# Kernel tuning notes

Hardware: AMD Instinct MI355X
Metric: run time of the kernel (lower is better)

Reference implementation:

```python
import jax, jax.numpy as jnp
import numpy as np

B, C, P, T = 256, 248, 50, 4
H = 8
D = C // H          # 31, used for the attention scale (self.d ** -0.5)
DH = D * T          # 124 == dim_head of RelPosEmb1DAISummer
FFD = 16
EPS = 1e-5


def _bn(x, g, b):
    # BatchNorm2d with batch statistics over (N, H, W) per channel
    m = x.mean(axis=(0, 2, 3), keepdims=True)
    v = x.var(axis=(0, 2, 3), keepdims=True)
    return (x - m) * jax.lax.rsqrt(v + EPS) * g[None, :, None, None] + b[None, :, None, None]


def _conv(x, w, b, pw):
    # kernel is (1, kw): 'same' padding only along the last (t) axis
    y = jax.lax.conv_general_dilated(x, w, (1, 1), ((0, 0), (pw, pw)),
                                     dimension_numbers=('NCHW', 'OIHW', 'NCHW'))
    return y + b[None, :, None, None]


def _rel_to_abs(x):
    # x: [b, h, l, 2l-1] -> [b, h, l, l] (Bottleneck-Transformer trick)
    b, h, l, _ = x.shape
    x = jnp.pad(x, ((0, 0), (0, 0), (0, 0), (0, 1)))           # b h l 2l
    x = x.reshape(b, h, 2 * l * l)
    x = jnp.pad(x, ((0, 0), (0, 0), (0, l - 1)))
    x = x.reshape(b, h, l + 1, 2 * l - 1)
    return x[:, :, :l, l - 1:]


def _forward(x, w_qkv, b_qkv, rel_emb, g1, beta1, w_c1, bc1, w_c2, bc2,
             g_cfe, beta_cfe, w_c3, bc3, g2, beta2):
    b, c, p, t = x.shape
    h, d = H, c // H
    dh = d * t
    # 1x1 conv qkv projection
    qkv = jnp.einsum('bcpt,oc->bopt', x, w_qkv) + b_qkv[None, :, None, None]
    qkv = qkv.reshape(b, 3, h, d, p, t)
    q = qkv[:, 0].transpose(0, 1, 3, 2, 4).reshape(b, h, p, dh)   # b h p (d t)
    k = qkv[:, 1].transpose(0, 1, 2, 4, 3).reshape(b, h, dh, p)   # b h (d t) p
    v = qkv[:, 2].transpose(0, 1, 3, 2, 4).reshape(b, h, p, dh)
    dots = jnp.matmul(q, k)                                       # b h p p
    bias = _rel_to_abs(jnp.einsum('bhpd,rd->bhpr', q, rel_emb))   # shared-head rel bias
    attn = jax.nn.softmax((dots + bias) * (d ** -0.5), axis=-1)   # scale AFTER bias, d=31
    out = jnp.matmul(attn, v)                                     # b h p dh
    out = out.reshape(b, h, p, d, t).transpose(0, 1, 3, 2, 4).reshape(b, c, p, t)
    # residual + BN1
    x = _bn(out + x, g1, beta1)
    # CFE: two parallel convs, concat, BN, ELU, 1x1 conv (dropout = identity, eval)
    y = jnp.concatenate([_conv(x, w_c1, bc1, 1), _conv(x, w_c2, bc2, 2)], axis=1)
    y = jax.nn.elu(_bn(y, g_cfe, beta_cfe))
    y = _conv(y, w_c3, bc3, 0)
    # residual + BN2
    return _bn(y + x, g2, beta2)


def setup_inputs() -> dict:
    key = jax.random.key(0)
    ks = jax.random.split(key, 8)
    rn = lambda k, sh, s=1.0: jax.random.normal(k, sh, dtype=jnp.float32) * s
    return dict(
        x=rn(ks[0], (B, C, P, T)),
        w_qkv=rn(ks[1], (3 * C, C), 0.05), b_qkv=jnp.zeros((3 * C,), jnp.float32),
        rel_emb=rn(ks[2], (2 * P - 1, DH), DH ** -0.5),
        g1=jnp.ones((C,), jnp.float32), beta1=jnp.zeros((C,), jnp.float32),
        w_c1=rn(ks[3], (FFD // 2, C, 1, 3), 0.05), bc1=jnp.zeros((FFD // 2,), jnp.float32),
        w_c2=rn(ks[4], (FFD // 2, C, 1, 5), 0.05), bc2=jnp.zeros((FFD // 2,), jnp.float32),
        g_cfe=jnp.ones((FFD,), jnp.float32), beta_cfe=jnp.zeros((FFD,), jnp.float32),
        w_c3=rn(ks[5], (C, FFD, 1, 1), 0.05), bc3=jnp.zeros((C,), jnp.float32),
        g2=jnp.ones((C,), jnp.float32), beta2=jnp.zeros((C,), jnp.float32),
    )


def reference(x, w_qkv, b_qkv, rel_emb, g1, beta1, w_c1, bc1, w_c2, bc2,
              g_cfe, beta_cfe, w_c3, bc3, g2, beta2):
    return _forward(x, w_qkv, b_qkv, rel_emb, g1, beta1, w_c1, bc1, w_c2, bc2,
                    g_cfe, beta_cfe, w_c3, bc3, g2, beta2)
```

## Files before the change

kernel.cpp:

```cpp
#include <hip/hip_runtime.h>

#define B_ 256
#define C_ 248
#define P_ 50
#define T_ 4
#define H_ 8
#define D_ 31
#define DH_ 124
#define PT_ 200
#define O3_ 744

typedef __attribute__((ext_vector_type(8))) short short8v;
typedef __attribute__((ext_vector_type(4))) float f32x4;

__device__ __forceinline__ float bf2f(unsigned short u) {
  union { unsigned int i; float f; } v; v.i = ((unsigned int)u) << 16; return v.f;
}
__device__ __forceinline__ unsigned short f2bf(float f) {
  union { float f; unsigned int i; } v; v.f = f;
  unsigned int r = v.i + 0x7fffu + ((v.i >> 16) & 1u);
  return (unsigned short)(r >> 16);
}

__global__ void relcvt_kernel(const float* __restrict__ rel, unsigned short* __restrict__ out) {
  int i = blockIdx.x * 256 + threadIdx.x;
  if (i < 112 * 128) {
    int r = i >> 7, k = i & 127;
    out[i] = (r < 99 && k < DH_) ? f2bf(rel[r * DH_ + k]) : (unsigned short)0;
  }
}

__global__ void wcvt_kernel(const float* __restrict__ w, unsigned short* __restrict__ wbf) {
  int i = blockIdx.x * 256 + threadIdx.x;
  if (i < 768 * 64) {
    int o = i >> 6, c = (i & 63) * 4;
    ushort4 val = make_ushort4(0, 0, 0, 0);
    if (o < O3_ && c < C_) {
      float4 wv = *(const float4*)(w + (size_t)o * C_ + c);
      val.x = f2bf(wv.x); val.y = f2bf(wv.y); val.z = f2bf(wv.z); val.w = f2bf(wv.w);
    }
    *(ushort4*)(wbf + (size_t)o * 256 + c) = val;
  }
}

__global__ __launch_bounds__(256) void xt_kernel(const float* __restrict__ x,
                                                 unsigned short* __restrict__ xT) {
  __shared__ float xs[64 * 65];
  const int tid = threadIdx.x;
  const int pt0 = (blockIdx.x & 3) * 64;
  const int c0 = (blockIdx.x >> 2) * 64;
  const int b = blockIdx.y;
#pragma unroll
  for (int pass = 0; pass < 4; ++pass) {
    int row = pass * 16 + (tid >> 4);
    int ptl4 = (tid & 15) * 4;
    int c = c0 + row, pt = pt0 + ptl4;
    float4 v = make_float4(0.f, 0.f, 0.f, 0.f);
    if (c < C_) {
      const float* src = x + ((size_t)b * C_ + c) * PT_ + pt;
      if (pt + 3 < PT_) v = *(const float4*)src;
      else {
        if (pt + 0 < PT_) v.x = src[0];
        if (pt + 1 < PT_) v.y = src[1];
        if (pt + 2 < PT_) v.z = src[2];
        if (pt + 3 < PT_) v.w = src[3];
      }
    }
    xs[row * 65 + ptl4 + 0] = v.x; xs[row * 65 + ptl4 + 1] = v.y;
    xs[row * 65 + ptl4 + 2] = v.z; xs[row * 65 + ptl4 + 3] = v.w;
  }
  __syncthreads();
#pragma unroll
  for (int pass = 0; pass < 4; ++pass) {
    int ptl = pass * 16 + (tid >> 4);
    int cl4 = (tid & 15) * 4;
    int pt = pt0 + ptl;
    if (pt < 208) {
      ushort4 pk;
      pk.x = f2bf(xs[(cl4 + 0) * 65 + ptl]);
      pk.y = f2bf(xs[(cl4 + 1) * 65 + ptl]);
      pk.z = f2bf(xs[(cl4 + 2) * 65 + ptl]);
      pk.w = f2bf(xs[(cl4 + 3) * 65 + ptl]);
      *(ushort4*)(xT + ((size_t)b * 208 + pt) * 256 + c0 + cl4) = pk;
    }
  }
}

__global__ __launch_bounds__(256) void fused_qa_kernel(
    const unsigned short* __restrict__ xT, const unsigned short* __restrict__ wbf,
    const float* __restrict__ bias, const unsigned short* __restrict__ relp,
    const float* __restrict__ x, float* __restrict__ pre1) {
  __shared__ __align__(16) unsigned short RA[64 * 128];
  __shared__ __align__(16) unsigned short RB[64 * 128];
  __shared__ __align__(16) unsigned short RC[128 * 64];
  const int tid = threadIdx.x;
  const int xcd = blockIdx.x & 7, slot = blockIdx.x >> 3;
  const int b = xcd * 32 + (slot >> 3), h = slot & 7;
  const unsigned short* xb = xT + (size_t)b * 208 * 256;
  const int w = tid >> 6, l = tid & 63;
  const int lr = l & 15, lk = (l >> 4) * 8;
  const int mstart = (w == 0) ? 0 : (1 + 3 * w);
  const int mcount = (w == 0) ? 4 : 3;
  const float scale = 0.17960530202677491f;

  {
    float4 z = make_float4(0.f, 0.f, 0.f, 0.f);
    float4* z1 = (float4*)RA; float4* z2 = (float4*)RB; float4* z3 = (float4*)RC;
    for (int i = tid; i < 1024; i += 256) { z1[i] = z; z2[i] = z; z3[i] = z; }
  }

  const f32x4 zf = {0.f, 0.f, 0.f, 0.f};
  f32x4 acc[4][6];
#pragma unroll
  for (int mi = 0; mi < 4; ++mi)
#pragma unroll
    for (int nt = 0; nt < 6; ++nt) acc[mi][nt] = zf;

#pragma unroll
  for (int ks = 0; ks < 8; ++ks) {
    int k0 = ks * 32 + lk;
    short8v bfr[6];
#pragma unroll
    for (int nt = 0; nt < 6; ++nt) {
      int orow = (nt >> 1) * 248 + h * 31 + (nt & 1) * 16 + lr;
      bfr[nt] = *(const short8v*)(wbf + (size_t)orow * 256 + k0);
    }
#pragma unroll
    for (int mi = 0; mi < 4; ++mi) {
      if (mi < mcount) {
        short8v a = *(const short8v*)(xb + (size_t)((mstart + mi) * 16 + lr) * 256 + k0);
#pragma unroll
        for (int nt = 0; nt < 6; ++nt)
          acc[mi][nt] = __builtin_amdgcn_mfma_f32_16x16x32_bf16(a, bfr[nt], acc[mi][nt], 0, 0, 0);
      }
    }
  }
  __syncthreads();
#pragma unroll
  for (int mi = 0; mi < 4; ++mi) {
    if (mi < mcount) {
      int p = (mstart + mi) * 4 + (l >> 4);
      if (p < P_) {
#pragma unroll
        for (int nt = 0; nt < 6; ++nt) {
          int d = (nt & 1) * 16 + lr;
          if (d < D_) {
            int wi = nt >> 1;
            float bo = bias[wi * C_ + h * D_ + d];
            f32x4 av = acc[mi][nt];
            if (wi == 2) {
#pragma unroll
              for (int r = 0; r < 4; ++r) {
                int dh = d * 4 + r;
                *(unsigned short*)((char*)RC + ((dh * 128 + p * 2) ^ ((dh & 7) << 4))) = f2bf(av[0] + bo);
                av = __builtin_shufflevector(av, av, 1, 2, 3, 0);
              }
            } else if (wi == 0) {
              ushort4 pk;
              pk.x = f2bf((av[0] + bo) * scale); pk.y = f2bf((av[1] + bo) * scale);
              pk.z = f2bf((av[2] + bo) * scale); pk.w = f2bf((av[3] + bo) * scale);
              *(ushort4*)((char*)RA + ((p * 256 + d * 8) ^ ((p & 7) << 4))) = pk;
            } else {
              ushort4 pk;
              pk.x = f2bf(av[0] + bo); pk.y = f2bf(av[1] + bo);
              pk.z = f2bf(av[2] + bo); pk.w = f2bf(av[3] + bo);
              *(ushort4*)((char*)RB + ((p * 256 + d * 8) ^ ((p & 7) << 4))) = pk;
            }
          }
        }
      }
    }
  }
  __syncthreads();

  const int arow = 16 * w + lr;
  const int prow0 = 16 * w + (l >> 4) * 4;

  f32x4 accS[4]; f32x4 accR[7];
#pragma unroll
  for (int n = 0; n < 4; ++n) accS[n] = zf;
#pragma unroll
  for (int n = 0; n < 7; ++n) accR[n] = zf;

#pragma unroll
  for (int ks = 0; ks < 4; ++ks) {
    int k0 = ks * 32 + lk;
    short8v a = *(const short8v*)((const char*)RA + ((arow * 256 + 2 * k0) ^ ((arow & 7) << 4)));
#pragma unroll
    for (int n = 0; n < 4; ++n) {
      int brow = 16 * n + lr;
      short8v bb = *(const short8v*)((const char*)RB + ((brow * 256 + 2 * k0) ^ ((brow & 7) << 4)));
      accS[n] = __builtin_amdgcn_mfma_f32_16x16x32_bf16(a, bb, accS[n], 0, 0, 0);
    }
#pragma unroll
    for (int n = 0; n < 7; ++n) {
      int rrow = 16 * n + lr;
      short8v bb = *(const short8v*)(relp + rrow * 128 + k0);
      accR[n] = __builtin_amdgcn_mfma_f32_16x16x32_bf16(a, bb, accR[n], 0, 0, 0);
    }
  }
  __syncthreads();

  unsigned short* bias_s = RB;
#pragma unroll
  for (int n = 0; n < 7; ++n)
#pragma unroll
    for (int r = 0; r < 4; ++r) {
      int p = prow0 + r;
      int j = 16 * n + lr - 49 + p;
      if (p < P_ && j >= 0 && j < P_)
        bias_s[p * 64 + j] = f2bf(accR[n][r]);
    }
  __syncthreads();

  float sv[4][4];
#pragma unroll
  for (int n = 0; n < 4; ++n)
#pragma unroll
    for (int r = 0; r < 4; ++r) {
      int p = prow0 + r, j = 16 * n + lr;
      if (p < P_ && j < P_)
        sv[n][r] = accS[n][r] + bf2f(bias_s[p * 64 + j]);
      else
        sv[n][r] = -1e30f;
    }
#pragma unroll
  for (int r = 0; r < 4; ++r) {
    float mm = fmaxf(fmaxf(sv[0][r], sv[1][r]), fmaxf(sv[2][r], sv[3][r]));
    mm = fmaxf(mm, __shfl_xor(mm, 1));
    mm = fmaxf(mm, __shfl_xor(mm, 2));
    mm = fmaxf(mm, __shfl_xor(mm, 4));
    mm = fmaxf(mm, __shfl_xor(mm, 8));
    float ss = 0.f;
#pragma unroll
    for (int n = 0; n < 4; ++n) { float e = __expf(sv[n][r] - mm); sv[n][r] = e; ss += e; }
    ss += __shfl_xor(ss, 1); ss += __shfl_xor(ss, 2);
    ss += __shfl_xor(ss, 4); ss += __shfl_xor(ss, 8);
    float inv = 1.f / ss;
#pragma unroll
    for (int n = 0; n < 4; ++n) sv[n][r] *= inv;
  }
#pragma unroll
  for (int n = 0; n < 4; ++n)
#pragma unroll
    for (int r = 0; r < 4; ++r) {
      int p = prow0 + r, j = 16 * n + lr;
      *(unsigned short*)((char*)RA + ((p * 128 + 2 * j) ^ ((p & 7) << 4))) = f2bf(sv[n][r]);
    }
  __syncthreads();

  f32x4 accO[8];
#pragma unroll
  for (int n = 0; n < 8; ++n) accO[n] = zf;
#pragma unroll
  for (int ks = 0; ks < 2; ++ks) {
    int j0 = ks * 32 + lk;
    short8v a = *(const short8v*)((const char*)RA + ((arow * 128 + 2 * j0) ^ ((arow & 7) << 4)));
#pragma unroll
    for (int n = 0; n < 8; ++n) {
      int vrow = 16 * n + lr;
      short8v bb = *(const short8v*)((const char*)RC + ((vrow * 128 + 2 * j0) ^ ((vrow & 7) << 4)));
      accO[n] = __builtin_amdgcn_mfma_f32_16x16x32_bf16(a, bb, accO[n], 0, 0, 0);
    }
  }
#pragma unroll
  for (int n = 0; n < 8; ++n) {
    int dh = 16 * n + lr;
    if (dh < DH_) {
      int c = h * D_ + (dh >> 2), t = dh & 3;
#pragma unroll
      for (int r = 0; r < 4; ++r) {
        int p = prow0 + r;
        if (p < P_) {
          size_t idx = (((size_t)b * C_ + c) * P_ + p) * T_ + t;
          pre1[idx] = accO[n][r] + x[idx];
        }
      }
    }
  }
}

__global__ __launch_bounds__(256) void bnstat_kernel(
    const float* __restrict__ t, const float* __restrict__ g, const float* __restrict__ be,
    float* __restrict__ a, float* __restrict__ bs, int nch) {
  const int c = blockIdx.x;
  const int tid = threadIdx.x;
  const float* base = t + ((size_t)tid * nch + c) * PT_;
  float s = 0.f, s2 = 0.f;
  for (int i = 0; i < PT_; i += 4) {
    float4 v = *(const float4*)(base + i);
    s += v.x + v.y + v.z + v.w;
    s2 += v.x*v.x + v.y*v.y + v.z*v.z + v.w*v.w;
  }
#pragma unroll
  for (int off = 32; off > 0; off >>= 1) {
    s += __shfl_down(s, off);
    s2 += __shfl_down(s2, off);
  }
  __shared__ float r1[4], r2[4];
  if ((tid & 63) == 0) { r1[tid>>6] = s; r2[tid>>6] = s2; }
  __syncthreads();
  if (tid == 0) {
    s = r1[0]+r1[1]+r1[2]+r1[3];
    s2 = r2[0]+r2[1]+r2[2]+r2[3];
    const float inv = 1.f / (float)(B_ * PT_);
    float m = s * inv;
    float var = s2 * inv - m * m;
    float ai = g[c] * rsqrtf(var + 1e-5f);
    a[c] = ai;
    bs[c] = be[c] - m * ai;
  }
}

__global__ __launch_bounds__(256) void p1t_kernel(const float* __restrict__ pre1,
                                                  unsigned short* __restrict__ p1T) {
  __shared__ float xs[64][205];
  const int b = blockIdx.x;
  const int tid = threadIdx.x;
  for (int c0 = 0; c0 < C_; c0 += 64) {
    int R = (C_ - c0 < 64) ? (C_ - c0) : 64;
    __syncthreads();
    for (int e = tid; e < R * 50; e += 256) {
      int row = e / 50, pq = e - (e / 50) * 50;
      float4 v = *(const float4*)(pre1 + ((size_t)b * C_ + c0 + row) * PT_ + pq * 4);
      xs[row][pq*4+0]=v.x; xs[row][pq*4+1]=v.y; xs[row][pq*4+2]=v.z; xs[row][pq*4+3]=v.w;
    }
    __syncthreads();
    for (int u = tid; u < 50 * R; u += 256) {
      int p = u / R, cl = u - (u / R) * R;
      ushort4 pk;
      pk.x = f2bf(xs[cl][p*4+0]); pk.y = f2bf(xs[cl][p*4+1]);
      pk.z = f2bf(xs[cl][p*4+2]); pk.w = f2bf(xs[cl][p*4+3]);
      *(ushort4*)(p1T + ((size_t)b*50 + p) * 1024 + (c0+cl)*4) = pk;
    }
  }
  for (int u = tid; u < 50 * 8; u += 256) {
    int p = u >> 3, g = u & 7;
    ushort4 val = make_ushort4(0,0,0,0);
    if (g == 0) val.x = 0x3F80;
    *(ushort4*)(p1T + ((size_t)b*50 + p) * 1024 + 992 + g*4) = val;
  }
}

__global__ __launch_bounds__(256) void wcfe_kernel(
    const float* __restrict__ w1, const float* __restrict__ bc1,
    const float* __restrict__ w2, const float* __restrict__ bc2,
    const float* __restrict__ a1, const float* __restrict__ b1,
    unsigned short* __restrict__ Wbig) {
  const int n = blockIdx.x;
  const int f = n >> 2, t = n & 3;
  const int tid = threadIdx.x;
  __shared__ float red[256];
  float partial = 0.f;
  if (tid < C_) {
    int c = tid;
    float tv[4];
    float tsum = 0.f;
#pragma unroll
    for (int tp = 0; tp < 4; ++tp) {
      int dt = tp - t;
      float v = 0.f;
      if (f < 8) { if (dt >= -1 && dt <= 1) v = w1[(f * C_ + c) * 3 + dt + 1]; }
      else       { if (dt >= -2 && dt <= 2) v = w2[((f - 8) * C_ + c) * 5 + dt + 2]; }
      tv[tp] = v; tsum += v;
    }
    float ac = a1[c];
#pragma unroll
    for (int tp = 0; tp < 4; ++tp)
      Wbig[n * 1024 + c * 4 + tp] = f2bf(ac * tv[tp]);
    partial = b1[c] * tsum;
  } else {
#pragma unroll
    for (int tp = 0; tp < 4; ++tp) {
      int col = tid * 4 + tp;
      if (col > 992 && col < 1024) Wbig[n * 1024 + col] = 0;
    }
  }
  red[tid] = partial;
  __syncthreads();
  for (int s = 128; s > 0; s >>= 1) {
    if (tid < s) red[tid] += red[tid + s];
    __syncthreads();
  }
  if (tid == 0) {
    float bias = (f < 8) ? bc1[f] : bc2[f - 8];
    Wbig[n * 1024 + 992] = f2bf(bias + red[0]);
  }
}

__global__ __launch_bounds__(256) void cfe12g_kernel(
    const unsigned short* __restrict__ p1T, const unsigned short* __restrict__ Wbig,
    float* __restrict__ y16) {
  const int tid = threadIdx.x;
  const int w = tid >> 6, l = tid & 63;
  const int lr = l & 15, lk = (l >> 4) * 8;
  const int m0 = blockIdx.x * 32;
  const f32x4 zf = {0.f, 0.f, 0.f, 0.f};
  f32x4 acc0 = zf, acc1 = zf;
  const unsigned short* wrow = Wbig + (size_t)(w * 16 + lr) * 1024;
#pragma unroll
  for (int ks = 0; ks < 32; ++ks) {
    int k0 = ks * 32 + lk;
    short8v bfr = *(const short8v*)(wrow + k0);
    short8v a0 = *(const short8v*)(p1T + (size_t)(m0 + lr) * 1024 + k0);
    short8v a1v = *(const short8v*)(p1T + (size_t)(m0 + 16 + lr) * 1024 + k0);
    acc0 = __builtin_amdgcn_mfma_f32_16x16x32_bf16(a0, bfr, acc0, 0, 0, 0);
    acc1 = __builtin_amdgcn_mfma_f32_16x16x32_bf16(a1v, bfr, acc1, 0, 0, 0);
  }
  const int n = w * 16 + lr, f = n >> 2, tt = n & 3;
#pragma unroll
  for (int mt = 0; mt < 2; ++mt) {
    f32x4 av = (mt == 0) ? acc0 : acc1;
#pragma unroll
    for (int r = 0; r < 4; ++r) {
      int m = m0 + mt * 16 + (l >> 4) * 4 + r;
      int b = m / 50, p = m - (m / 50) * 50;
      y16[((size_t)b * 16 + f) * PT_ + p * 4 + tt] = av[r];
    }
  }
}

__global__ __launch_bounds__(256) void cfe3_kernel(
    const float* __restrict__ y16, const float* __restrict__ ac, const float* __restrict__ bcf,
    const float* __restrict__ w3, const float* __restrict__ bc3,
    const float* __restrict__ pre1, const float* __restrict__ a1, const float* __restrict__ b1,
    float* __restrict__ pre2) {
  const int b = blockIdx.x;
  const int tid = threadIdx.x;
  __shared__ float zs[16][PT_];
  __shared__ float w3s[C_][16];
  for (int i = tid; i < C_*16; i += 256) w3s[i >> 4][i & 15] = w3[i];
  for (int e = tid; e < 16*PT_; e += 256) {
    int f = e / PT_, pt = e - f * PT_;
    float v = y16[((size_t)b*16 + f) * PT_ + pt] * ac[f] + bcf[f];
    zs[f][pt] = (v > 0.f) ? v : (__expf(v) - 1.f);
  }
  __syncthreads();
  for (int e = tid; e < C_ * P_; e += 256) {
    int c = e / P_, p = e - (e / P_) * P_;
    float b3 = bc3[c];
    float4 o = make_float4(b3, b3, b3, b3);
#pragma unroll
    for (int f = 0; f < 16; ++f) {
      float wv = w3s[c][f];
      float4 z = *(const float4*)&zs[f][p*4];
      o.x += wv * z.x; o.y += wv * z.y; o.z += wv * z.z; o.w += wv * z.w;
    }
    size_t idx = (((size_t)b * C_ + c) * P_ + p) * T_;
    float4 xr = *(const float4*)(pre1 + idx);
    float a1c = a1[c], b1c = b1[c];
    o.x += xr.x * a1c + b1c;
    o.y += xr.y * a1c + b1c;
    o.z += xr.z * a1c + b1c;
    o.w += xr.w * a1c + b1c;
    *(float4*)(pre2 + idx) = o;
  }
}

__global__ __launch_bounds__(256) void bnapply_kernel(
    const float* __restrict__ pre2, const float* __restrict__ a, const float* __restrict__ bs,
    float* __restrict__ out) {
  int i = blockIdx.x * 256 + threadIdx.x;
  if (i < (B_*C_*PT_)/4) {
    int row = (i * 4) / PT_;
    int c = row % C_;
    float4 v = *(const float4*)(pre2 + (size_t)i * 4);
    float ai = a[c], bi = bs[c];
    float4 o = make_float4(v.x*ai+bi, v.y*ai+bi, v.z*ai+bi, v.w*ai+bi);
    *(float4*)(out + (size_t)i * 4) = o;
  }
}

extern "C" void kernel_launch(void* const* d_in, const int* in_sizes, int n_in,
                              void* d_out, int out_size, void* d_ws, size_t ws_size,
                              hipStream_t stream) {
  const float* x        = (const float*)d_in[0];
  const float* w_qkv    = (const float*)d_in[1];
  const float* b_qkv    = (const float*)d_in[2];
  const float* rel      = (const float*)d_in[3];
  const float* g1       = (const float*)d_in[4];
  const float* beta1    = (const float*)d_in[5];
  const float* w_c1     = (const float*)d_in[6];
  const float* bc1      = (const float*)d_in[7];
  const float* w_c2     = (const float*)d_in[8];
  const float* bc2      = (const float*)d_in[9];
  const float* g_cfe    = (const float*)d_in[10];
  const float* beta_cfe = (const float*)d_in[11];
  const float* w_c3     = (const float*)d_in[12];
  const float* bc3      = (const float*)d_in[13];
  const float* g2       = (const float*)d_in[14];
  const float* beta2    = (const float*)d_in[15];
  float* out = (float*)d_out;
  char* ws = (char*)d_ws;

  unsigned short* xT    = (unsigned short*)(ws);
  unsigned short* wbf   = (unsigned short*)(ws + 27262976);
  unsigned short* p1T   = (unsigned short*)(ws + 27656192);
  float* pre1           = (float*)(ws + 76185600);
  float* y16            = (float*)(ws + 126976000);
  unsigned short* relp  = (unsigned short*)(ws + 130252800);
  unsigned short* Wbig  = (unsigned short*)(ws + 130281472);
  float* st             = (float*)(ws + 130412544);
  float* a1 = st, *b1 = st + 256, *acf = st + 512, *bcf = st + 544, *a2 = st + 576, *b2 = st + 832;
  float* pre2           = (float*)ws;

  relcvt_kernel<<<56, 256, 0, stream>>>(rel, relp);
  wcvt_kernel<<<192, 256, 0, stream>>>(w_qkv, wbf);
  xt_kernel<<<dim3(16, 256), 256, 0, stream>>>(x, xT);
  fused_qa_kernel<<<2048, 256, 0, stream>>>(xT, wbf, b_qkv, relp, x, pre1);
  bnstat_kernel<<<248, 256, 0, stream>>>(pre1, g1, beta1, a1, b1, C_);
  p1t_kernel<<<256, 256, 0, stream>>>(pre1, p1T);
  wcfe_kernel<<<64, 256, 0, stream>>>(w_c1, bc1, w_c2, bc2, a1, b1, Wbig);
  cfe12g_kernel<<<400, 256, 0, stream>>>(p1T, Wbig, y16);
  bnstat_kernel<<<16, 256, 0, stream>>>(y16, g_cfe, beta_cfe, acf, bcf, 16);
  cfe3_kernel<<<256, 256, 0, stream>>>(y16, acf, bcf, w_c3, bc3, pre1, a1, b1, pre2);
  bnstat_kernel<<<248, 256, 0, stream>>>(pre2, g2, beta2, a2, b2, C_);
  bnapply_kernel<<<12400, 256, 0, stream>>>(pre2, a2, b2, out);
}
```

Measured before the change: 397.8 us.

## Fuse BN1 stats and bf16 transpose into attention epilogue, split BN reductions

The attention kernel now writes its residual output straight into the bf16 transposed buffer and accumulates per-channel sum and sum-of-squares partials. This removes the fp32 pre1 tensor, the separate transpose kernel and the full BN1 statistics pass. cfe3 reads the residual back from the bf16 buffer instead of fp32, which lowers the precision of the residual path. The remaining BN statistics passes are split into a partial-reduction kernel over more blocks plus a small finalize kernel, to get more parallelism. The epilogue's stores are scattered 2-byte writes, which may coalesce poorly.

```diff
diff --git a/kernel.cpp b/kernel.cpp
--- a/kernel.cpp
+++ b/kernel.cpp
@@ -89,7 +89,8 @@
 __global__ __launch_bounds__(256) void fused_qa_kernel(
     const unsigned short* __restrict__ xT, const unsigned short* __restrict__ wbf,
     const float* __restrict__ bias, const unsigned short* __restrict__ relp,
-    const float* __restrict__ x, float* __restrict__ pre1) {
+    const float* __restrict__ x, unsigned short* __restrict__ p1T,
+    float* __restrict__ partial1) {
   __shared__ __align__(16) unsigned short RA[64 * 128];
   __shared__ __align__(16) unsigned short RB[64 * 128];
   __shared__ __align__(16) unsigned short RC[128 * 64];
@@ -263,6 +264,9 @@
       accO[n] = __builtin_amdgcn_mfma_f32_16x16x32_bf16(a, bb, accO[n], 0, 0, 0);
     }
   }
+  float psum[8], psq[8];
+#pragma unroll
+  for (int n = 0; n < 8; ++n) { psum[n] = 0.f; psq[n] = 0.f; }
 #pragma unroll
   for (int n = 0; n < 8; ++n) {
     int dh = 16 * n + lr;
@@ -272,37 +276,66 @@
       for (int r = 0; r < 4; ++r) {
         int p = prow0 + r;
         if (p < P_) {
-          size_t idx = (((size_t)b * C_ + c) * P_ + p) * T_ + t;
-          pre1[idx] = accO[n][r] + x[idx];
+          float val = accO[n][r] + x[(((size_t)b * C_ + c) * P_ + p) * T_ + t];
+          p1T[((size_t)b * 50 + p) * 1024 + h * DH_ + dh] = f2bf(val);
+          psum[n] += val;
+          psq[n] += val * val;
         }
       }
     }
   }
-}
-
-__global__ __launch_bounds__(256) void bnstat_kernel(
-    const float* __restrict__ t, const float* __restrict__ g, const float* __restrict__ be,
-    float* __restrict__ a, float* __restrict__ bs, int nch) {
+#pragma unroll
+  for (int n = 0; n < 8; ++n) {
+    psum[n] += __shfl_xor(psum[n], 1);  psq[n] += __shfl_xor(psq[n], 1);
+    psum[n] += __shfl_xor(psum[n], 2);  psq[n] += __shfl_xor(psq[n], 2);
+    psum[n] += __shfl_xor(psum[n], 16); psq[n] += __shfl_xor(psq[n], 16);
+    psum[n] += __shfl_xor(psum[n], 32); psq[n] += __shfl_xor(psq[n], 32);
+  }
+  float* fs = (float*)RB;
+  if ((l & 3) == 0 && l < 16) {
+    int g2 = l >> 2;
+#pragma unroll
+    for (int n = 0; n < 8; ++n) {
+      int d = 4 * n + g2;
+      if (d < D_) { fs[w * 32 + d] = psum[n]; fs[128 + w * 32 + d] = psq[n]; }
+    }
+  }
+  __syncthreads();
+  if (tid < D_) {
+    float s = fs[tid] + fs[32 + tid] + fs[64 + tid] + fs[96 + tid];
+    float s2 = fs[128 + tid] + fs[160 + tid] + fs[192 + tid] + fs[224 + tid];
+    partial1[((size_t)b * 8 + h) * 62 + tid] = s;
+    partial1[((size_t)b * 8 + h) * 62 + 31 + tid] = s2;
+  }
+  if (h == 7) {
+    for (int u = tid; u < 400; u += 256) {
+      int p = u >> 3, g3 = u & 7;
+      ushort4 vz = make_ushort4(0, 0, 0, 0);
+      if (g3 == 0) vz.x = 0x3F80;
+      *(ushort4*)(p1T + ((size_t)b * 50 + p) * 1024 + 992 + g3 * 4) = vz;
+    }
+  }
+}
+
+__global__ __launch_bounds__(256) void bnfin1_kernel(
+    const float* __restrict__ partial1, const float* __restrict__ g,
+    const float* __restrict__ be, float* __restrict__ a, float* __restrict__ bs) {
   const int c = blockIdx.x;
-  const int tid = threadIdx.x;
-  const float* base = t + ((size_t)tid * nch + c) * PT_;
-  float s = 0.f, s2 = 0.f;
-  for (int i = 0; i < PT_; i += 4) {
-    float4 v = *(const float4*)(base + i);
-    s += v.x + v.y + v.z + v.w;
-    s2 += v.x*v.x + v.y*v.y + v.z*v.z + v.w*v.w;
-  }
-#pragma unroll
-  for (int off = 32; off > 0; off >>= 1) {
-    s += __shfl_down(s, off);
-    s2 += __shfl_down(s2, off);
+  const int h = c / D_, d = c - h * D_;
+  const int tid = threadIdx.x;
+  const float* pp = partial1 + ((size_t)tid * 8 + h) * 62;
+  float s = pp[d], s2 = pp[31 + d];
+#pragma unroll
+  for (int off = 1; off <= 32; off <<= 1) {
+    s += __shfl_xor(s, off);
+    s2 += __shfl_xor(s2, off);
   }
   __shared__ float r1[4], r2[4];
-  if ((tid & 63) == 0) { r1[tid>>6] = s; r2[tid>>6] = s2; }
+  if ((tid & 63) == 0) { r1[tid >> 6] = s; r2[tid >> 6] = s2; }
   __syncthreads();
   if (tid == 0) {
-    s = r1[0]+r1[1]+r1[2]+r1[3];
-    s2 = r2[0]+r2[1]+r2[2]+r2[3];
+    s = r1[0] + r1[1] + r1[2] + r1[3];
+    s2 = r2[0] + r2[1] + r2[2] + r2[3];
     const float inv = 1.f / (float)(B_ * PT_);
     float m = s * inv;
     float var = s2 * inv - m * m;
@@ -312,33 +345,52 @@
   }
 }
 
-__global__ __launch_bounds__(256) void p1t_kernel(const float* __restrict__ pre1,
-                                                  unsigned short* __restrict__ p1T) {
-  __shared__ float xs[64][205];
-  const int b = blockIdx.x;
-  const int tid = threadIdx.x;
-  for (int c0 = 0; c0 < C_; c0 += 64) {
-    int R = (C_ - c0 < 64) ? (C_ - c0) : 64;
-    __syncthreads();
-    for (int e = tid; e < R * 50; e += 256) {
-      int row = e / 50, pq = e - (e / 50) * 50;
-      float4 v = *(const float4*)(pre1 + ((size_t)b * C_ + c0 + row) * PT_ + pq * 4);
-      xs[row][pq*4+0]=v.x; xs[row][pq*4+1]=v.y; xs[row][pq*4+2]=v.z; xs[row][pq*4+3]=v.w;
-    }
-    __syncthreads();
-    for (int u = tid; u < 50 * R; u += 256) {
-      int p = u / R, cl = u - (u / R) * R;
-      ushort4 pk;
-      pk.x = f2bf(xs[cl][p*4+0]); pk.y = f2bf(xs[cl][p*4+1]);
-      pk.z = f2bf(xs[cl][p*4+2]); pk.w = f2bf(xs[cl][p*4+3]);
-      *(ushort4*)(p1T + ((size_t)b*50 + p) * 1024 + (c0+cl)*4) = pk;
-    }
-  }
-  for (int u = tid; u < 50 * 8; u += 256) {
-    int p = u >> 3, g = u & 7;
-    ushort4 val = make_ushort4(0,0,0,0);
-    if (g == 0) val.x = 0x3F80;
-    *(ushort4*)(p1T + ((size_t)b*50 + p) * 1024 + 992 + g*4) = val;
+__global__ __launch_bounds__(256) void bnstat_part_kernel(
+    const float* __restrict__ t, float* __restrict__ part, int nch) {
+  const int c = blockIdx.x, g = blockIdx.y;
+  const int tid = threadIdx.x;
+  const int bsl = tid >> 3, k = tid & 7;
+  const int b = g * 32 + bsl;
+  const float* base = t + ((size_t)b * nch + c) * PT_;
+  float s = 0.f, s2 = 0.f;
+  for (int j = k; j < 50; j += 8) {
+    float4 v = *(const float4*)(base + j * 4);
+    s += v.x + v.y + v.z + v.w;
+    s2 += v.x * v.x + v.y * v.y + v.z * v.z + v.w * v.w;
+  }
+#pragma unroll
+  for (int off = 1; off <= 32; off <<= 1) {
+    s += __shfl_xor(s, off);
+    s2 += __shfl_xor(s2, off);
+  }
+  __shared__ float r1[4], r2[4];
+  if ((tid & 63) == 0) { r1[tid >> 6] = s; r2[tid >> 6] = s2; }
+  __syncthreads();
+  if (tid == 0) {
+    s = r1[0] + r1[1] + r1[2] + r1[3];
+    s2 = r2[0] + r2[1] + r2[2] + r2[3];
+    part[((size_t)c * 8 + g) * 2] = s;
+    part[((size_t)c * 8 + g) * 2 + 1] = s2;
+  }
+}
+
+__global__ __launch_bounds__(256) void bnfin_kernel(
+    const float* __restrict__ part, const float* __restrict__ g,
+    const float* __restrict__ be, float* __restrict__ a, float* __restrict__ bs, int nch) {
+  int c = threadIdx.x;
+  if (c < nch) {
+    float s = 0.f, s2 = 0.f;
+#pragma unroll
+    for (int gg = 0; gg < 8; ++gg) {
+      s += part[((size_t)c * 8 + gg) * 2];
+      s2 += part[((size_t)c * 8 + gg) * 2 + 1];
+    }
+    const float inv = 1.f / (float)(B_ * PT_);
+    float m = s * inv;
+    float var = s2 * inv - m * m;
+    float ai = g[c] * rsqrtf(var + 1e-5f);
+    a[c] = ai;
+    bs[c] = be[c] - m * ai;
   }
 }
 
@@ -423,16 +475,16 @@
 __global__ __launch_bounds__(256) void cfe3_kernel(
     const float* __restrict__ y16, const float* __restrict__ ac, const float* __restrict__ bcf,
     const float* __restrict__ w3, const float* __restrict__ bc3,
-    const float* __restrict__ pre1, const float* __restrict__ a1, const float* __restrict__ b1,
+    const unsigned short* __restrict__ p1T, const float* __restrict__ a1, const float* __restrict__ b1,
     float* __restrict__ pre2) {
   const int b = blockIdx.x;
   const int tid = threadIdx.x;
   __shared__ float zs[16][PT_];
   __shared__ float w3s[C_][16];
-  for (int i = tid; i < C_*16; i += 256) w3s[i >> 4][i & 15] = w3[i];
-  for (int e = tid; e < 16*PT_; e += 256) {
+  for (int i = tid; i < C_ * 16; i += 256) w3s[i >> 4][i & 15] = w3[i];
+  for (int e = tid; e < 16 * PT_; e += 256) {
     int f = e / PT_, pt = e - f * PT_;
-    float v = y16[((size_t)b*16 + f) * PT_ + pt] * ac[f] + bcf[f];
+    float v = y16[((size_t)b * 16 + f) * PT_ + pt] * ac[f] + bcf[f];
     zs[f][pt] = (v > 0.f) ? v : (__expf(v) - 1.f);
   }
   __syncthreads();
@@ -443,16 +495,16 @@
 #pragma unroll
     for (int f = 0; f < 16; ++f) {
       float wv = w3s[c][f];
-      float4 z = *(const float4*)&zs[f][p*4];
+      float4 z = *(const float4*)&zs[f][p * 4];
       o.x += wv * z.x; o.y += wv * z.y; o.z += wv * z.z; o.w += wv * z.w;
     }
+    ushort4 xr = *(const ushort4*)(p1T + ((size_t)(b * 50 + p)) * 1024 + c * 4);
+    float a1c = a1[c], b1c = b1[c];
+    o.x += bf2f(xr.x) * a1c + b1c;
+    o.y += bf2f(xr.y) * a1c + b1c;
+    o.z += bf2f(xr.z) * a1c + b1c;
+    o.w += bf2f(xr.w) * a1c + b1c;
     size_t idx = (((size_t)b * C_ + c) * P_ + p) * T_;
-    float4 xr = *(const float4*)(pre1 + idx);
-    float a1c = a1[c], b1c = b1[c];
-    o.x += xr.x * a1c + b1c;
-    o.y += xr.y * a1c + b1c;
-    o.z += xr.z * a1c + b1c;
-    o.w += xr.w * a1c + b1c;
     *(float4*)(pre2 + idx) = o;
   }
 }
@@ -461,12 +513,12 @@
     const float* __restrict__ pre2, const float* __restrict__ a, const float* __restrict__ bs,
     float* __restrict__ out) {
   int i = blockIdx.x * 256 + threadIdx.x;
-  if (i < (B_*C_*PT_)/4) {
+  if (i < (B_ * C_ * PT_) / 4) {
     int row = (i * 4) / PT_;
     int c = row % C_;
     float4 v = *(const float4*)(pre2 + (size_t)i * 4);
     float ai = a[c], bi = bs[c];
-    float4 o = make_float4(v.x*ai+bi, v.y*ai+bi, v.z*ai+bi, v.w*ai+bi);
+    float4 o = make_float4(v.x * ai + bi, v.y * ai + bi, v.z * ai + bi, v.w * ai + bi);
     *(float4*)(out + (size_t)i * 4) = o;
   }
 }
@@ -496,24 +548,27 @@
   unsigned short* xT    = (unsigned short*)(ws);
   unsigned short* wbf   = (unsigned short*)(ws + 27262976);
   unsigned short* p1T   = (unsigned short*)(ws + 27656192);
-  float* pre1           = (float*)(ws + 76185600);
+  float* part2          = (float*)(ws + 53870592);
+  float* partY          = (float*)(ws + 53886464);
+  float* pre2           = (float*)(ws + 76185600);
   float* y16            = (float*)(ws + 126976000);
+  float* partial1       = (float*)(ws + 126976000);
   unsigned short* relp  = (unsigned short*)(ws + 130252800);
   unsigned short* Wbig  = (unsigned short*)(ws + 130281472);
   float* st             = (float*)(ws + 130412544);
   float* a1 = st, *b1 = st + 256, *acf = st + 512, *bcf = st + 544, *a2 = st + 576, *b2 = st + 832;
-  float* pre2           = (float*)ws;
 
   relcvt_kernel<<<56, 256, 0, stream>>>(rel, relp);
   wcvt_kernel<<<192, 256, 0, stream>>>(w_qkv, wbf);
   xt_kernel<<<dim3(16, 256), 256, 0, stream>>>(x, xT);
-  fused_qa_kernel<<<2048, 256, 0, stream>>>(xT, wbf, b_qkv, relp, x, pre1);
-  bnstat_kernel<<<248, 256, 0, stream>>>(pre1, g1, beta1, a1, b1, C_);
-  p1t_kernel<<<256, 256, 0, stream>>>(pre1, p1T);
+  fused_qa_kernel<<<2048, 256, 0, stream>>>(xT, wbf, b_qkv, relp, x, p1T, partial1);
+  bnfin1_kernel<<<248, 256, 0, stream>>>(partial1, g1, beta1, a1, b1);
   wcfe_kernel<<<64, 256, 0, stream>>>(w_c1, bc1, w_c2, bc2, a1, b1, Wbig);
   cfe12g_kernel<<<400, 256, 0, stream>>>(p1T, Wbig, y16);
-  bnstat_kernel<<<16, 256, 0, stream>>>(y16, g_cfe, beta_cfe, acf, bcf, 16);
-  cfe3_kernel<<<256, 256, 0, stream>>>(y16, acf, bcf, w_c3, bc3, pre1, a1, b1, pre2);
-  bnstat_kernel<<<248, 256, 0, stream>>>(pre2, g2, beta2, a2, b2, C_);
+  bnstat_part_kernel<<<dim3(16, 8), 256, 0, stream>>>(y16, partY, 16);
+  bnfin_kernel<<<1, 256, 0, stream>>>(partY, g_cfe, beta_cfe, acf, bcf, 16);
+  cfe3_kernel<<<256, 256, 0, stream>>>(y16, acf, bcf, w_c3, bc3, p1T, a1, b1, pre2);
+  bnstat_part_kernel<<<dim3(248, 8), 256, 0, stream>>>(pre2, part2, 248);
+  bnfin_kernel<<<1, 256, 0, stream>>>(part2, g2, beta2, a2, b2, 248);
   bnapply_kernel<<<12400, 256, 0, stream>>>(pre2, a2, b2, out);
 }
```

Result: faster. 367.0 us (-7.7%).
